# Optimization experiments

Hardware: AMD Instinct MI355X
Metric: run time of the kernel (lower is better)

## Reference

```python
import jax, jax.numpy as jnp
import numpy as np

BN_EPS = 1e-5


def gcn_conv(x, src, dst, W, b):
    # PyG GCNConv: add self-loops, symmetric normalization, bias after aggregation
    n = x.shape[0]
    h = x @ W                                   # [N, d]
    deg = jnp.zeros((n,), x.dtype).at[dst].add(1.0) + 1.0  # in-degree + self-loop
    dinv = jax.lax.rsqrt(deg)
    norm = dinv[src] * dinv[dst]                # [E]
    agg = jnp.zeros_like(h).at[dst].add(h[src] * norm[:, None])
    agg = agg + h * (dinv * dinv)[:, None]      # self-loop messages
    return agg + b


def batchnorm(x, gamma, beta):
    mu = x.mean(0)
    var = x.var(0)  # biased, as torch BN training mode
    return (x - mu) * jax.lax.rsqrt(var + BN_EPS) * gamma + beta


def mha(x, w_in, b_in, w_out, b_out, n_heads=4):
    # torch nn.MultiheadAttention, input [L, N, E]
    L, N, d = x.shape
    hd = d // n_heads
    qkv = x @ w_in.T + b_in                     # [L, N, 3d]
    q, k, v = jnp.split(qkv, 3, axis=-1)
    rh = lambda t: t.reshape(L, N, n_heads, hd)
    q = rh(q) * (1.0 / np.sqrt(hd))
    k, v = rh(k), rh(v)
    scores = jnp.einsum('lnhd,mnhd->nhlm', q, k)
    a = jax.nn.softmax(scores, axis=-1)
    o = jnp.einsum('nhlm,mnhd->lnhd', a, v).reshape(L, N, d)
    return o @ w_out.T + b_out


def setup_inputs() -> dict:
    key = jax.random.key(0)
    N, d, E, L, R = 50000, 128, 400000, 3, 4
    ks = jax.random.split(key, 12)
    s = 1.0 / np.sqrt(d)
    return {
        'features': jax.random.normal(ks[0], (N, d), jnp.float32),
        'rel_emb': jax.random.normal(ks[1], (R, d), jnp.float32),
        'edge_index': jax.random.randint(ks[2], (R, 2, E), 0, N, dtype=jnp.int32),
        'W_gcn': jax.random.normal(ks[3], (L, d, d), jnp.float32) * s,
        'b_gcn': jnp.zeros((L, d), jnp.float32),
        'bn_gamma': jnp.ones((L - 1, d), jnp.float32),
        'bn_beta': jnp.zeros((L - 1, d), jnp.float32),
        'W_rt': jax.random.normal(ks[4], (L, d, d), jnp.float32) * s,
        'b_rt': jnp.zeros((L, d), jnp.float32),
        'attn_w_in': jax.random.normal(ks[5], (3 * d, d), jnp.float32) * s,
        'attn_b_in': jnp.zeros((3 * d,), jnp.float32),
        'attn_w_out': jax.random.normal(ks[6], (d, d), jnp.float32) * s,
        'attn_b_out': jnp.zeros((d,), jnp.float32),
        'alphas': jnp.full((4,), 0.95, jnp.float32),
        'fusion_q': jax.random.normal(ks[7], (d,), jnp.float32),
        'fusion_w': jax.random.normal(ks[8], (d, d), jnp.float32) * s,
        'fusion_b': jnp.zeros((d,), jnp.float32),
    }


def reference(features, rel_emb, edge_index, W_gcn, b_gcn, bn_gamma, bn_beta,
              W_rt, b_rt, attn_w_in, attn_b_in, attn_w_out, attn_b_out,
              alphas, fusion_q, fusion_w, fusion_b):
    L = W_gcn.shape[0]
    # RelationGCN unpacks rel_emb as (poi_r, s_r, d_r, n_r) and processes
    # relations in order (n, poi, s, d) -> permute to processing order.
    perm = jnp.array([3, 0, 1, 2])
    rels = rel_emb[perm]                # [4, d], order (n, poi, s, d)
    edges = edge_index[perm]            # [4, 2, E]
    embs = jnp.broadcast_to(features, (4,) + features.shape)  # all start at features

    def inner(emb, r, src, dst, Wg, bg, gamma, beta):
        h = gcn_conv(emb * r, src, dst, Wg, bg)
        return emb + jax.nn.leaky_relu(batchnorm(h, gamma, beta))

    for i in range(L - 1):
        embs = jax.vmap(inner, in_axes=(0, 0, 0, 0, None, None, None, None))(
            embs, rels, edges[:, 0], edges[:, 1],
            W_gcn[i], b_gcn[i], bn_gamma[i], bn_beta[i])
        rels = rels @ W_rt[i].T + b_rt[i]
        # dropout p=0.0 -> identity

    embs = jax.vmap(lambda e, r, s_, t_: gcn_conv(e * r, s_, t_, W_gcn[-1], b_gcn[-1]))(
        embs, rels, edges[:, 0], edges[:, 1])
    rels = rels @ W_rt[-1].T + b_rt[-1]

    # PM_Model mis-unpacks RelationGCN outputs (returned order n,poi,s,d as
    # poi,s,d,n). CrossLayer then stacks (n_emb, poi_emb, d_emb, s_emb) which in
    # true processing order is (d, n, s, poi):
    stk = jnp.stack([embs[3], embs[0], embs[2], embs[1]])  # [4, N, d]
    fusion = mha(stk, attn_w_in, attn_b_in, attn_w_out, attn_b_out)
    a = alphas  # [alpha_n, alpha_poi, alpha_d, alpha_s]
    n_f = fusion[0] * a[0] + (1 - a[0]) * stk[0]
    poi_f = fusion[1] * a[1] + (1 - a[1]) * stk[1]
    d_f = fusion[2] * a[2] + (1 - a[2]) * stk[2]
    s_f = fusion[3] * a[3] + (1 - a[3]) * stk[3]

    def score(f):
        return jnp.mean(jnp.sum(jax.nn.leaky_relu(f @ fusion_w.T + fusion_b) * fusion_q, axis=1))

    w = jax.nn.softmax(jnp.stack([score(n_f), score(poi_f), score(s_f), score(d_f)]))
    region = w[0] * n_f + w[1] * poi_f + w[2] * s_f + w[3] * d_f

    # Final multiplies use the same mis-unpacked rel names:
    # n_r<-rels[3](true d), poi_r<-rels[0](true n), s_r<-rels[1], d_r<-rels[2]
    return (region, region * rels[3], region * rels[0], region * rels[1], region * rels[2])
```

## Files before the change

### kernel.cpp

```cpp
#include <hip/hip_runtime.h>
#include <cstdio>

#define DD 128
#define NREL 4

using short8 = __attribute__((ext_vector_type(8))) short;
using f32x4  = __attribute__((ext_vector_type(4))) float;

struct PtrB4 { const unsigned short* p[4]; };
struct OutB4 { unsigned short* p[4]; };

__device__ __forceinline__ int edge_perm(int r) { return (r + 3) & 3; }

__device__ __forceinline__ float bf_lo(unsigned u) { return __uint_as_float(u << 16); }
__device__ __forceinline__ float bf_hi(unsigned u) { return __uint_as_float(u & 0xffff0000u); }
__device__ __forceinline__ float bfe(short s) {
  return __uint_as_float(((unsigned)(unsigned short)s) << 16);
}
__device__ __forceinline__ unsigned short f2bf(float f) {
  unsigned x = __float_as_uint(f);
  unsigned r = (x + 0x7fffu + ((x >> 16) & 1u)) >> 16;
  return (unsigned short)r;
}
__device__ __forceinline__ unsigned pack2(float a, float b) {
  return (unsigned)f2bf(a) | ((unsigned)f2bf(b) << 16);
}


__global__ void rels_init(const float* __restrict__ rel_emb, float* __restrict__ rels) {
  int t = threadIdx.x;
  int r = t >> 7, c = t & 127;
  rels[t] = rel_emb[edge_perm(r) * DD + c];
}

__global__ void rels_update(const float* __restrict__ rin, const float* __restrict__ Wrt,
                            const float* __restrict__ brt, float* __restrict__ rout) {
  int t = threadIdx.x;
  int r = t >> 7, j = t & 127;
  float s = brt[j];
  const float* wr = Wrt + j * DD;
  const float* xr = rin + r * DD;
  for (int c = 0; c < DD; ++c) s += xr[c] * wr[c];
  rout[t] = s;
}

__global__ void scale_w_bf(const float* __restrict__ rels_i, const float* __restrict__ Wg,
                           unsigned short* __restrict__ Wsb) {
  int i = blockIdx.x * 256 + threadIdx.x;
  int r = i >> 14, rem = i & 16383, j = rem >> 7, c = rem & 127;
  Wsb[i] = f2bf(rels_i[r * DD + c] * Wg[c * DD + j]);
}

__global__ void conv_w(const float* __restrict__ w_in, const float* __restrict__ w_out,
                       const float* __restrict__ w_fus, unsigned short* __restrict__ Wab) {
  int i = blockIdx.x * 256 + threadIdx.x;
  float v = (i < 49152) ? w_in[i] : (i < 65536 ? w_out[i - 49152] : w_fus[i - 65536]);
  Wab[i] = f2bf(v);
}

__global__ void conv_f2b(const float* __restrict__ in, unsigned* __restrict__ out2, size_t n4) {
  size_t i = (size_t)blockIdx.x * 256 + threadIdx.x;
  if (i < n4) {
    float4 v = ((const float4*)in)[i];
    out2[i * 2]     = pack2(v.x, v.y);
    out2[i * 2 + 1] = pack2(v.z, v.w);
  }
}


__global__ void count_deg(const int* __restrict__ ei, int* __restrict__ deg, int N, int E) {
  int r = blockIdx.y;
  int base = blockIdx.x * 1024 + threadIdx.x;
  const int* dsts = ei + (size_t)edge_perm(r) * 2 * E + E;
#pragma unroll
  for (int k = 0; k < 4; ++k) {
    int e = base + k * 256;
    if (e < E) atomicAdd(deg + (size_t)r * N + dsts[e], 1);
  }
}

__global__ void finalize_dinv(const int* __restrict__ deg, float* __restrict__ dinv, int total) {
  int i = blockIdx.x * 256 + threadIdx.x;
  if (i < total) dinv[i] = rsqrtf((float)deg[i] + 1.0f);
}

__global__ void scan_block(const int* __restrict__ deg, int* __restrict__ excl,
                           int* __restrict__ bsums, int n) {
  __shared__ int sh[256];
  int i = blockIdx.x * 256 + threadIdx.x;
  int v = (i < n) ? deg[i] : 0;
  sh[threadIdx.x] = v;
  __syncthreads();
  for (int st = 1; st < 256; st <<= 1) {
    int t = (threadIdx.x >= st) ? sh[threadIdx.x - st] : 0;
    __syncthreads();
    sh[threadIdx.x] += t;
    __syncthreads();
  }
  if (i < n) excl[i] = sh[threadIdx.x] - v;
  if (threadIdx.x == 255) bsums[blockIdx.x] = sh[255];
}

__global__ void scan_sums(int* __restrict__ bsums, int nb) {
  __shared__ int sh[1024];
  int v = (threadIdx.x < nb) ? bsums[threadIdx.x] : 0;
  sh[threadIdx.x] = v;
  __syncthreads();
  for (int st = 1; st < 1024; st <<= 1) {
    int t = (threadIdx.x >= st) ? sh[threadIdx.x - st] : 0;
    __syncthreads();
    sh[threadIdx.x] += t;
    __syncthreads();
  }
  if (threadIdx.x < nb) bsums[threadIdx.x] = sh[threadIdx.x] - v;
}

__global__ void scan_add(int* __restrict__ excl, int* __restrict__ cursor,
                         const int* __restrict__ bsums, int n) {
  int i = blockIdx.x * 256 + threadIdx.x;
  if (i < n) {
    int o = excl[i] + bsums[blockIdx.x];
    excl[i] = o;
    cursor[i] = o;
  }
}

__global__ void fill_edges(const int* __restrict__ ei, int* __restrict__ cursor,
                           int* __restrict__ srcbuf, int N, int E) {
  int r = blockIdx.y;
  int base = blockIdx.x * 1024 + threadIdx.x;
  const int* bp = ei + (size_t)edge_perm(r) * 2 * E;
  int s[4], d[4], pos[4];
#pragma unroll
  for (int k = 0; k < 4; ++k) {
    int e = base + k * 256;
    s[k] = (e < E) ? bp[e] : 0;
    d[k] = (e < E) ? bp[E + e] : 0;
  }
#pragma unroll
  for (int k = 0; k < 4; ++k) {
    int e = base + k * 256;
    if (e < E) pos[k] = atomicAdd(&cursor[r * N + d[k]], 1);
  }
#pragma unroll
  for (int k = 0; k < 4; ++k) {
    int e = base + k * 256;
    if (e < E) srcbuf[pos[k]] = r * N + s[k];
  }
}

template <int MODE>
__global__ __launch_bounds__(256) void gemm_ws(PtrB4 xs, PtrB4 wz, OutB4 ys,
                                               const float* __restrict__ bias,
                                               const float* __restrict__ dinv,
                                               const float* __restrict__ fq,
                                               float* __restrict__ S,
                                               PtrB4 stks,
                                               const float* __restrict__ alphas,
                                               int M) {
  int z = blockIdx.y;
  const unsigned short* __restrict__ X = xs.p[z];
  const unsigned short* __restrict__ W = wz.p[z];
  int tid = threadIdx.x;
  int wave = tid >> 6, lane = tid & 63;
  int r16 = lane & 15, kgrp = lane >> 4;
  int rowhalf = wave >> 1, colbase = (wave & 1) * 64;
  int blockrow = blockIdx.x * 64;

  short8 b[4][4];
#pragma unroll
  for (int s = 0; s < 4; ++s)
#pragma unroll
    for (int cn = 0; cn < 4; ++cn)
      b[s][cn] = *(const short8*)(W + ((colbase + cn * 16 + r16) << 7) + s * 32 + kgrp * 8);

  int row0 = blockrow + rowhalf * 32 + r16;
  int r0c = row0 < M ? row0 : M - 1;
  int r1c = row0 + 16 < M ? row0 + 16 : M - 1;
  short8 a[2][4];
#pragma unroll
  for (int s = 0; s < 4; ++s) {
    a[0][s] = *(const short8*)(X + (size_t)r0c * DD + s * 32 + kgrp * 8);
    a[1][s] = *(const short8*)(X + (size_t)r1c * DD + s * 32 + kgrp * 8);
  }

  f32x4 acc[2][4];
#pragma unroll
  for (int rt = 0; rt < 2; ++rt)
#pragma unroll
    for (int cn = 0; cn < 4; ++cn)
#pragma unroll
      for (int j = 0; j < 4; ++j) acc[rt][cn][j] = 0.f;

#pragma unroll
  for (int s = 0; s < 4; ++s)
#pragma unroll
    for (int rt = 0; rt < 2; ++rt)
#pragma unroll
      for (int cn = 0; cn < 4; ++cn)
        acc[rt][cn] = __builtin_amdgcn_mfma_f32_16x16x32_bf16(a[rt][s], b[s][cn], acc[rt][cn], 0, 0, 0);

  __shared__ float red[256];
  if constexpr (MODE == 2) {
    float ss = 0.f;
#pragma unroll
    for (int rt = 0; rt < 2; ++rt)
#pragma unroll
      for (int cn = 0; cn < 4; ++cn) {
        int col = colbase + cn * 16 + r16;
        float bb = bias[col];
        float qc = fq[col];
#pragma unroll
        for (int i = 0; i < 4; ++i) {
          int row = blockrow + rowhalf * 32 + rt * 16 + kgrp * 4 + i;
          if (row < M) {
            float y = acc[rt][cn][i] + bb;
            float v = y > 0.f ? y : 0.01f * y;
            ss += v * qc;
          }
        }
      }
    red[tid] = ss;
    __syncthreads();
    for (int st = 128; st > 0; st >>= 1) {
      if (tid < st) red[tid] += red[tid + st];
      __syncthreads();
    }
    if (tid == 0) atomicAdd(S + z, red[0]);
  } else {
    __shared__ __align__(16) unsigned short tile[64][DD + 8];
    float dv[2][4];
    if constexpr (MODE == 0) {
#pragma unroll
      for (int rt = 0; rt < 2; ++rt)
#pragma unroll
        for (int i = 0; i < 4; ++i) {
          int row = blockrow + rowhalf * 32 + rt * 16 + kgrp * 4 + i;
          dv[rt][i] = dinv[(size_t)z * M + (row < M ? row : 0)];
        }
    }
#pragma unroll
    for (int rt = 0; rt < 2; ++rt)
#pragma unroll
      for (int cn = 0; cn < 4; ++cn) {
        int col = colbase + cn * 16 + r16;
        float bb = (MODE == 1 || MODE == 3) ? bias[col] : 0.f;
#pragma unroll
        for (int i = 0; i < 4; ++i) {
          int wrow = rowhalf * 32 + rt * 16 + kgrp * 4 + i;
          float y = acc[rt][cn][i] + bb;
          if constexpr (MODE == 0) y *= dv[rt][i];
          tile[wrow][col] = f2bf(y);
        }
      }
    __syncthreads();
    int orow = tid >> 2, seg = tid & 3;
    int grow = blockrow + orow;
    if (grow < M) {
      unsigned short* Yp = ys.p[z] + (size_t)grow * DD + seg * 32;
      const unsigned short* tp = &tile[orow][seg * 32];
      if constexpr (MODE == 3) {
        float aa = alphas[z], na = 1.f - aa;
        const unsigned short* sp = stks.p[z] + (size_t)grow * DD + seg * 32;
#pragma unroll
        for (int k = 0; k < 4; ++k) {
          uint4 pv = *(const uint4*)(tp + k * 8);
          uint4 sv = *(const uint4*)(sp + k * 8);
          const unsigned* pw = &pv.x;
          const unsigned* sw = &sv.x;
          uint4 o; unsigned* ow = &o.x;
#pragma unroll
          for (int j = 0; j < 4; ++j)
            ow[j] = pack2(aa * bf_lo(pw[j]) + na * bf_lo(sw[j]),
                          aa * bf_hi(pw[j]) + na * bf_hi(sw[j]));
          *(uint4*)(Yp + k * 8) = o;
        }
      } else {
#pragma unroll
        for (int k = 0; k < 4; ++k)
          *(uint4*)(Yp + k * 8) = *(const uint4*)(tp + k * 8);
      }
    }
  }
}

template <int WB>
__global__ __launch_bounds__(256) void gemm_upd(PtrB4 res, PtrB4 abs_, PtrB4 wz,
                                                OutB4 xout, OutB4 ys,
                                                const float* __restrict__ ssx,
                                                const float* __restrict__ dinv, int M) {
  int z = blockIdx.y;
  const unsigned short* __restrict__ R = res.p[z];
  const unsigned short* __restrict__ A = abs_.p[z];
  const unsigned short* __restrict__ W = wz.p[z];
  int tid = threadIdx.x;

  __shared__ float ssc[DD], ssh[DD];
  if (tid < DD) {
    ssc[tid] = ssx[((size_t)z * DD + tid) * 2];
    ssh[tid] = ssx[((size_t)z * DD + tid) * 2 + 1];
  }
  __syncthreads();

  int wave = tid >> 6, lane = tid & 63;
  int r16 = lane & 15, kgrp = lane >> 4;
  int rowhalf = wave >> 1, colbase = (wave & 1) * 64;
  int blockrow = blockIdx.x * 64;

  short8 b[4][4];
#pragma unroll
  for (int s = 0; s < 4; ++s)
#pragma unroll
    for (int cn = 0; cn < 4; ++cn)
      b[s][cn] = *(const short8*)(W + ((colbase + cn * 16 + r16) << 7) + s * 32 + kgrp * 8);

  int row0 = blockrow + rowhalf * 32 + r16;
  int rc[2];
  rc[0] = row0 < M ? row0 : M - 1;
  rc[1] = row0 + 16 < M ? row0 + 16 : M - 1;
  short8 a[2][4];
#pragma unroll
  for (int rt = 0; rt < 2; ++rt)
#pragma unroll
    for (int s = 0; s < 4; ++s) {
      int cbase = s * 32 + kgrp * 8;
      short8 rv = *(const short8*)(R + (size_t)rc[rt] * DD + cbase);
      short8 av = *(const short8*)(A + (size_t)rc[rt] * DD + cbase);
      short8 av2;
#pragma unroll
      for (int j = 0; j < 8; ++j) {
        float x = bfe(av[j]) * ssc[cbase + j] + ssh[cbase + j];
        x = x > 0.f ? x : 0.01f * x;
        av2[j] = (short)f2bf(bfe(rv[j]) + x);
      }
      a[rt][s] = av2;
    }
  if (WB) {
#pragma unroll
    for (int rt = 0; rt < 2; ++rt) {
      int row = row0 + rt * 16;
      if (row < M) {
#pragma unroll
        for (int s = 0; s < 4; ++s)
          *(short8*)(xout.p[z] + (size_t)row * DD + s * 32 + kgrp * 8) = a[rt][s];
      }
    }
  }

  f32x4 acc[2][4];
#pragma unroll
  for (int rt = 0; rt < 2; ++rt)
#pragma unroll
    for (int cn = 0; cn < 4; ++cn)
#pragma unroll
      for (int j = 0; j < 4; ++j) acc[rt][cn][j] = 0.f;
#pragma unroll
  for (int s = 0; s < 4; ++s)
#pragma unroll
    for (int rt = 0; rt < 2; ++rt)
#pragma unroll
      for (int cn = 0; cn < 4; ++cn)
        acc[rt][cn] = __builtin_amdgcn_mfma_f32_16x16x32_bf16(a[rt][s], b[s][cn], acc[rt][cn], 0, 0, 0);

  __shared__ __align__(16) unsigned short tile[64][DD + 8];
  float dv[2][4];
#pragma unroll
  for (int rt = 0; rt < 2; ++rt)
#pragma unroll
    for (int i = 0; i < 4; ++i) {
      int row = blockrow + rowhalf * 32 + rt * 16 + kgrp * 4 + i;
      dv[rt][i] = dinv[(size_t)z * M + (row < M ? row : 0)];
    }
#pragma unroll
  for (int rt = 0; rt < 2; ++rt)
#pragma unroll
    for (int cn = 0; cn < 4; ++cn) {
      int col = colbase + cn * 16 + r16;
#pragma unroll
      for (int i = 0; i < 4; ++i) {
        int wrow = rowhalf * 32 + rt * 16 + kgrp * 4 + i;
        tile[wrow][col] = f2bf(acc[rt][cn][i] * dv[rt][i]);
      }
    }
  __syncthreads();
  int orow = tid >> 2, seg = tid & 3;
  int grow = blockrow + orow;
  if (grow < M) {
    unsigned short* Yp = ys.p[z] + (size_t)grow * DD + seg * 32;
    const unsigned short* tp = &tile[orow][seg * 32];
#pragma unroll
    for (int k = 0; k < 4; ++k)
      *(uint4*)(Yp + k * 8) = *(const uint4*)(tp + k * 8);
  }
}

__global__ __launch_bounds__(256) void gather_agg(const int* __restrict__ srcbuf,
                                                  const int* __restrict__ offs,
                                                  const int* __restrict__ deg,
                                                  const float* __restrict__ dinv,
                                                  const uint2* __restrict__ Bs2,
                                                  const float* __restrict__ bias,
                                                  uint2* __restrict__ Ab2, int N4) {
  int rn = blockIdx.x * 8 + (threadIdx.x >> 5);
  if (rn >= N4) return;
  int lane = threadIdx.x & 31;
  int st = offs[rn], cnt = deg[rn];
  uint2 u = Bs2[(size_t)rn * 32 + lane];
  float a0 = bf_lo(u.x), a1 = bf_hi(u.x), a2 = bf_lo(u.y), a3 = bf_hi(u.y);
  int e = 0;
  for (; e + 8 <= cnt; e += 8) {
    int rr[8];
#pragma unroll
    for (int j = 0; j < 8; ++j) rr[j] = srcbuf[st + e + j];
    uint2 vv[8];
#pragma unroll
    for (int j = 0; j < 8; ++j) vv[j] = Bs2[(size_t)rr[j] * 32 + lane];
#pragma unroll
    for (int j = 0; j < 8; ++j) {
      a0 += bf_lo(vv[j].x); a1 += bf_hi(vv[j].x);
      a2 += bf_lo(vv[j].y); a3 += bf_hi(vv[j].y);
    }
  }
  if (e + 4 <= cnt) {
    int rr[4];
#pragma unroll
    for (int j = 0; j < 4; ++j) rr[j] = srcbuf[st + e + j];
    uint2 vv[4];
#pragma unroll
    for (int j = 0; j < 4; ++j) vv[j] = Bs2[(size_t)rr[j] * 32 + lane];
#pragma unroll
    for (int j = 0; j < 4; ++j) {
      a0 += bf_lo(vv[j].x); a1 += bf_hi(vv[j].x);
      a2 += bf_lo(vv[j].y); a3 += bf_hi(vv[j].y);
    }
    e += 4;
  }
  for (; e < cnt; ++e) {
    uint2 v = Bs2[(size_t)srcbuf[st + e] * 32 + lane];
    a0 += bf_lo(v.x); a1 += bf_hi(v.x); a2 += bf_lo(v.y); a3 += bf_hi(v.y);
  }
  float dvv = dinv[rn];
  int c = lane * 4;
  uint2 o;
  o.x = pack2(a0 * dvv + bias[c],     a1 * dvv + bias[c + 1]);
  o.y = pack2(a2 * dvv + bias[c + 2], a3 * dvv + bias[c + 3]);
  Ab2[(size_t)rn * 32 + lane] = o;
}


__global__ void bn_stats(const unsigned* __restrict__ Ab2, float* __restrict__ sums, int N) {
  int r = blockIdx.y;
  int lane = threadIdx.x & 63, grp = threadIdx.x >> 6;
  float s0 = 0.f, q0 = 0.f, s1 = 0.f, q1 = 0.f;
  const unsigned* base = Ab2 + (size_t)r * N * 64;
  for (int n = blockIdx.x * 4 + grp; n < N; n += gridDim.x * 4) {
    unsigned u = base[(size_t)n * 64 + lane];
    float a = bf_lo(u), b = bf_hi(u);
    s0 += a; q0 += a * a; s1 += b; q1 += b * b;
  }
  __shared__ float sh[4][64][4];
  sh[grp][lane][0] = s0; sh[grp][lane][1] = q0; sh[grp][lane][2] = s1; sh[grp][lane][3] = q1;
  __syncthreads();
  if (grp == 0) {
#pragma unroll
    for (int g = 1; g < 4; ++g) {
      s0 += sh[g][lane][0]; q0 += sh[g][lane][1]; s1 += sh[g][lane][2]; q1 += sh[g][lane][3];
    }
    int c0 = lane * 2;
    atomicAdd(sums + (r * DD + c0) * 2, s0);
    atomicAdd(sums + (r * DD + c0) * 2 + 1, q0);
    atomicAdd(sums + (r * DD + c0 + 1) * 2, s1);
    atomicAdd(sums + (r * DD + c0 + 1) * 2 + 1, q1);
  }
}

__global__ void bn_final(const float* __restrict__ sums, const float* __restrict__ gamma,
                         const float* __restrict__ beta, float* __restrict__ ss, int N) {
  int t = threadIdx.x;
  int c = t & 127;
  float mu = sums[t * 2] / N;
  float var = sums[t * 2 + 1] / N - mu * mu;
  float sc = gamma[c] * rsqrtf(var + 1e-5f);
  ss[t * 2] = sc;
  ss[t * 2 + 1] = beta[c] - mu * sc;
}

__global__ void attn_fused(const unsigned short* __restrict__ Q,
                           const unsigned short* __restrict__ K,
                           const unsigned short* __restrict__ V,
                           unsigned* __restrict__ Ob2, int N) {
  int sb = threadIdx.x >> 6;
  int node = blockIdx.x * 4 + sb;
  int lane = threadIdx.x & 63;
  __shared__ float qs[4][4][132], ks[4][4][132], vs[4][4][132];
  __shared__ float ps[4][64];
  if (node < N) {
    int l = lane >> 4, c8 = (lane & 15) * 8;
    uint4 qv = *(const uint4*)(Q + ((size_t)l * N + node) * DD + c8);
    uint4 kv = *(const uint4*)(K + ((size_t)l * N + node) * DD + c8);
    uint4 vv = *(const uint4*)(V + ((size_t)l * N + node) * DD + c8);
    unsigned qa[4] = {qv.x, qv.y, qv.z, qv.w};
    unsigned ka[4] = {kv.x, kv.y, kv.z, kv.w};
    unsigned va[4] = {vv.x, vv.y, vv.z, vv.w};
#pragma unroll
    for (int j = 0; j < 4; ++j) {
      qs[sb][l][c8 + 2 * j]     = bf_lo(qa[j]);
      qs[sb][l][c8 + 2 * j + 1] = bf_hi(qa[j]);
      ks[sb][l][c8 + 2 * j]     = bf_lo(ka[j]);
      ks[sb][l][c8 + 2 * j + 1] = bf_hi(ka[j]);
      vs[sb][l][c8 + 2 * j]     = bf_lo(va[j]);
      vs[sb][l][c8 + 2 * j + 1] = bf_hi(va[j]);
    }
  }
  __syncthreads();
  if (node < N) {
    int h = lane >> 4, l = (lane >> 2) & 3, m = lane & 3;
    const float* qp = &qs[sb][l][h * 32];
    const float* kp = &ks[sb][m][h * 32];
    float s = 0.f;
#pragma unroll
    for (int k2 = 0; k2 < 32; ++k2) s += qp[k2] * kp[k2];
    s *= 0.17677669529663687f;
    float mx = s;
    mx = fmaxf(mx, __shfl_xor(mx, 1));
    mx = fmaxf(mx, __shfl_xor(mx, 2));
    float e = expf(s - mx);
    float sum = e;
    sum += __shfl_xor(sum, 1);
    sum += __shfl_xor(sum, 2);
    ps[sb][lane] = e / sum;
  }
  __syncthreads();
  if (node < N) {
    int c0 = lane * 2, h = c0 >> 5;
    const float* pp = &ps[sb][h * 16];
#pragma unroll
    for (int l = 0; l < 4; ++l) {
      float ol = pp[l * 4 + 0] * vs[sb][0][c0] + pp[l * 4 + 1] * vs[sb][1][c0] +
                 pp[l * 4 + 2] * vs[sb][2][c0] + pp[l * 4 + 3] * vs[sb][3][c0];
      float oh = pp[l * 4 + 0] * vs[sb][0][c0 + 1] + pp[l * 4 + 1] * vs[sb][1][c0 + 1] +
                 pp[l * 4 + 2] * vs[sb][2][c0 + 1] + pp[l * 4 + 3] * vs[sb][3][c0 + 1];
      Ob2[((size_t)l * N + node) * 64 + lane] = pack2(ol, oh);
    }
  }
}

__global__ void wcoef(const float* __restrict__ S, float* __restrict__ coef, int N) {
  if (threadIdx.x == 0) {
    float v0 = S[0] / N, v1 = S[1] / N, v2 = S[3] / N, v3 = S[2] / N;
    float mx = fmaxf(fmaxf(v0, v1), fmaxf(v2, v3));
    float e0 = expf(v0 - mx), e1 = expf(v1 - mx), e2 = expf(v2 - mx), e3 = expf(v3 - mx);
    float inv = 1.f / (e0 + e1 + e2 + e3);
    coef[0] = e0 * inv; coef[1] = e1 * inv; coef[2] = e3 * inv; coef[3] = e2 * inv;
  }
}

__device__ __forceinline__ float bfat(uint2 u, int j) {
  unsigned w = (j < 2) ? u.x : u.y;
  return (j & 1) ? bf_hi(w) : bf_lo(w);
}

__global__ void final_out(const unsigned short* __restrict__ fb, const float* __restrict__ coef,
                          const float* __restrict__ rels3, float* __restrict__ out, int N) {
  size_t NK = (size_t)N * DD;
  size_t i4 = (size_t)blockIdx.x * 256 + threadIdx.x;
  if (i4 >= NK / 4) return;
  size_t g = i4 * 4;
  int c = (int)(g & 127);
  float c0 = coef[0], c1 = coef[1], c2 = coef[2], c3 = coef[3];
  uint2 u0 = *(const uint2*)(fb + g);
  uint2 u1 = *(const uint2*)(fb + NK + g);
  uint2 u2 = *(const uint2*)(fb + 2 * NK + g);
  uint2 u3 = *(const uint2*)(fb + 3 * NK + g);
  float4 reg4, o1, o2, o3, o4;
  float* rp = &reg4.x; float* p1 = &o1.x; float* p2 = &o2.x; float* p3 = &o3.x; float* p4 = &o4.x;
#pragma unroll
  for (int j = 0; j < 4; ++j) {
    float region = c0 * bfat(u0, j) + c1 * bfat(u1, j) + c2 * bfat(u2, j) + c3 * bfat(u3, j);
    rp[j] = region;
    p1[j] = region * rels3[3 * DD + c + j];
    p2[j] = region * rels3[0 * DD + c + j];
    p3[j] = region * rels3[1 * DD + c + j];
    p4[j] = region * rels3[2 * DD + c + j];
  }
  *(float4*)(out + g) = reg4;
  *(float4*)(out + NK + g) = o1;
  *(float4*)(out + 2 * NK + g) = o2;
  *(float4*)(out + 3 * NK + g) = o3;
  *(float4*)(out + 4 * NK + g) = o4;
}


extern "C" void kernel_launch(void* const* d_in, const int* in_sizes, int n_in,
                              void* d_out, int out_size, void* d_ws, size_t ws_size,
                              hipStream_t stream) {
  const float* features  = (const float*)d_in[0];
  const float* rel_emb   = (const float*)d_in[1];
  const int*   edge_idx  = (const int*)d_in[2];
  const float* W_gcn     = (const float*)d_in[3];
  const float* b_gcn     = (const float*)d_in[4];
  const float* bn_gamma  = (const float*)d_in[5];
  const float* bn_beta   = (const float*)d_in[6];
  const float* W_rt      = (const float*)d_in[7];
  const float* b_rt      = (const float*)d_in[8];
  const float* attn_w_in = (const float*)d_in[9];
  const float* attn_b_in = (const float*)d_in[10];
  const float* attn_wout = (const float*)d_in[11];
  const float* attn_bout = (const float*)d_in[12];
  const float* alphas    = (const float*)d_in[13];
  const float* fusion_q  = (const float*)d_in[14];
  const float* fusion_w  = (const float*)d_in[15];
  const float* fusion_b  = (const float*)d_in[16];

  int N = in_sizes[0] / DD;
  int E = in_sizes[2] / (2 * NREL);
  size_t NK = (size_t)N * DD;
  int N4 = 4 * N;

  unsigned short* Xb = (unsigned short*)d_ws;
  unsigned short* Bs = Xb + 4 * NK;
  unsigned short* Ab = Bs + 4 * NK;
  unsigned short* Ub = Ab + 4 * NK;
  unsigned short* Fb = Ub + 4 * NK;
  float* dinv  = (float*)(Fb + NK);
  unsigned short* Wgcnb = (unsigned short*)(dinv + N4);
  unsigned short* Wab   = Wgcnb + 4 * DD * DD;
  float* rels  = (float*)(Wab + 5 * DD * DD);
  float* bnsum = rels + 4 * 512;
  float* bnss  = bnsum + 1024;
  float* S     = bnss + 1024;
  float* coef  = S + 4;
  int* deg_i   = (int*)(coef + 4);
  int* offs    = deg_i + N4;
  int* cur     = offs + N4;
  int* bsums   = cur + N4;
  int* srcb    = bsums + 1024;

  size_t needed = (size_t)((char*)(srcb + 4 * E) - (char*)d_ws);
  if (ws_size < needed) {
    fprintf(stderr, "kernel_launch: ws too small (%zu < %zu)\n", ws_size, needed);
    return;
  }

  int gemmGrid = (N + 63) / 64;
  int scanBlocks = (N4 + 255) / 256;
  int egrid4 = (E + 1023) / 1024;

  hipMemsetAsync(deg_i, 0, (size_t)N4 * sizeof(int), stream);
  count_deg<<<dim3(egrid4, 4), 256, 0, stream>>>(edge_idx, deg_i, N, E);
  finalize_dinv<<<scanBlocks, 256, 0, stream>>>(deg_i, dinv, N4);
  scan_block<<<scanBlocks, 256, 0, stream>>>(deg_i, offs, bsums, N4);
  scan_sums<<<1, 1024, 0, stream>>>(bsums, scanBlocks);
  scan_add<<<scanBlocks, 256, 0, stream>>>(offs, cur, bsums, N4);
  fill_edges<<<dim3(egrid4, 4), 256, 0, stream>>>(edge_idx, cur, srcb, N, E);

  rels_init<<<1, 512, 0, stream>>>(rel_emb, rels);
  conv_w<<<5 * 16384 / 256, 256, 0, stream>>>(attn_w_in, attn_wout, fusion_w, Wab);
  conv_f2b<<<(int)((NK / 4 + 255) / 256), 256, 0, stream>>>(features, (unsigned*)Fb, NK / 4);

  PtrB4 wz, abIn, resIn, dummyP;
  OutB4 msgOut, xbOut, dummyO;
  for (int r = 0; r < 4; ++r) {
    wz.p[r] = Wgcnb + (size_t)r * DD * DD;
    abIn.p[r] = Ab + (size_t)r * NK;
    msgOut.p[r] = Bs + (size_t)r * NK;
    xbOut.p[r] = Xb + (size_t)r * NK;
    dummyP.p[r] = nullptr;
    dummyO.p[r] = nullptr;
  }
  const float* dummy = nullptr;

  scale_w_bf<<<256, 256, 0, stream>>>(rels, W_gcn, Wgcnb);
  {
    PtrB4 xs; for (int r = 0; r < 4; ++r) xs.p[r] = Fb;
    gemm_ws<0><<<dim3(gemmGrid, 4), 256, 0, stream>>>(xs, wz, msgOut, dummy, dinv, dummy,
                                                      nullptr, dummyP, dummy, N);
  }
  gather_agg<<<(N4 + 7) / 8, 256, 0, stream>>>(srcb, offs, deg_i, dinv, (const uint2*)Bs,
                                               b_gcn, (uint2*)Ab, N4);
  hipMemsetAsync(bnsum, 0, 1024 * sizeof(float), stream);
  bn_stats<<<dim3(128, 4), 256, 0, stream>>>((const unsigned*)Ab, bnsum, N);
  bn_final<<<1, 512, 0, stream>>>(bnsum, bn_gamma, bn_beta, bnss, N);
  rels_update<<<1, 512, 0, stream>>>(rels, W_rt, b_rt, rels + 512);

  scale_w_bf<<<256, 256, 0, stream>>>(rels + 512, W_gcn + (size_t)DD * DD, Wgcnb);
  for (int r = 0; r < 4; ++r) resIn.p[r] = Fb;
  gemm_upd<1><<<dim3(gemmGrid, 4), 256, 0, stream>>>(resIn, abIn, wz, xbOut, msgOut,
                                                     bnss, dinv, N);
  gather_agg<<<(N4 + 7) / 8, 256, 0, stream>>>(srcb, offs, deg_i, dinv, (const uint2*)Bs,
                                               b_gcn + DD, (uint2*)Ab, N4);
  hipMemsetAsync(bnsum, 0, 1024 * sizeof(float), stream);
  bn_stats<<<dim3(128, 4), 256, 0, stream>>>((const unsigned*)Ab, bnsum, N);
  bn_final<<<1, 512, 0, stream>>>(bnsum, bn_gamma + DD, bn_beta + DD, bnss, N);
  rels_update<<<1, 512, 0, stream>>>(rels + 512, W_rt + (size_t)DD * DD, b_rt + DD, rels + 1024);

  scale_w_bf<<<256, 256, 0, stream>>>(rels + 1024, W_gcn + (size_t)2 * DD * DD, Wgcnb);
  for (int r = 0; r < 4; ++r) resIn.p[r] = Xb + (size_t)r * NK;
  gemm_upd<0><<<dim3(gemmGrid, 4), 256, 0, stream>>>(resIn, abIn, wz, dummyO, msgOut,
                                                     bnss, dinv, N);
  gather_agg<<<(N4 + 7) / 8, 256, 0, stream>>>(srcb, offs, deg_i, dinv, (const uint2*)Bs,
                                               b_gcn + 2 * DD, (uint2*)Ab, N4);
  rels_update<<<1, 512, 0, stream>>>(rels + 1024, W_rt + (size_t)2 * DD * DD, b_rt + 2 * DD,
                                     rels + 1536);

  const int pstk[4] = {3, 0, 2, 1};
  PtrB4 stk, fromO, fromF, w4;
  OutB4 toQ, toK, toV, toF;
  for (int l = 0; l < 4; ++l) {
    stk.p[l] = Ab + (size_t)pstk[l] * NK;
    toQ.p[l] = Xb + (size_t)l * NK;
    toK.p[l] = Bs + (size_t)l * NK;
    toV.p[l] = Ub + (size_t)l * NK;
    toF.p[l] = Bs + (size_t)l * NK;
    fromO.p[l] = Xb + (size_t)l * NK;
    fromF.p[l] = Bs + (size_t)l * NK;
  }

  for (int l = 0; l < 4; ++l) w4.p[l] = Wab;
  gemm_ws<1><<<dim3(gemmGrid, 4), 256, 0, stream>>>(stk, w4, toQ, attn_b_in, dummy, dummy,
                                                    nullptr, dummyP, dummy, N);
  for (int l = 0; l < 4; ++l) w4.p[l] = Wab + 16384;
  gemm_ws<1><<<dim3(gemmGrid, 4), 256, 0, stream>>>(stk, w4, toK, attn_b_in + DD, dummy, dummy,
                                                    nullptr, dummyP, dummy, N);
  for (int l = 0; l < 4; ++l) w4.p[l] = Wab + 2 * 16384;
  gemm_ws<1><<<dim3(gemmGrid, 4), 256, 0, stream>>>(stk, w4, toV, attn_b_in + 2 * DD, dummy,
                                                    dummy, nullptr, dummyP, dummy, N);
  attn_fused<<<(N + 3) / 4, 256, 0, stream>>>(Xb, Bs, Ub, (unsigned*)Xb, N);
  for (int l = 0; l < 4; ++l) w4.p[l] = Wab + 3 * 16384;
  gemm_ws<3><<<dim3(gemmGrid, 4), 256, 0, stream>>>(fromO, w4, toF, attn_bout, dummy, dummy,
                                                    nullptr, stk, alphas, N);
  hipMemsetAsync(S, 0, 4 * sizeof(float), stream);
  for (int l = 0; l < 4; ++l) w4.p[l] = Wab + 4 * 16384;
  gemm_ws<2><<<dim3(gemmGrid, 4), 256, 0, stream>>>(fromF, w4, toQ , fusion_b, dummy,
                                                    fusion_q, S, dummyP, dummy, N);
  wcoef<<<1, 64, 0, stream>>>(S, coef, N);
  final_out<<<(int)((NK / 4 + 255) / 256), 256, 0, stream>>>(Bs, coef, rels + 1536,
                                                             (float*)d_out, N);
}
```

Before: 1.031 ms.

## Stage GEMM weights in LDS and give each wave a full-width 16-row tile

Both GEMM kernels now copy the 128x128 bf16 weight tile into shared memory once per block with a padded row stride. Each wave then computes a 16x128 output slab, reading B fragments from LDS instead of holding a 64-column slice of B in registers. This cuts per-thread register use and the redundant global weight loads across waves, at the cost of LDS reads per MFMA and an extra barrier before the shared buffer is reused as the output tile. The bn_stats grid is also enlarged for more parallelism.

```diff
diff --git a/kernel.cpp b/kernel.cpp
--- a/kernel.cpp
+++ b/kernel.cpp
@@ -150,76 +150,75 @@
 }
 
 template <int MODE>
-__global__ __launch_bounds__(256) void gemm_ws(PtrB4 xs, PtrB4 wz, OutB4 ys,
-                                               const float* __restrict__ bias,
-                                               const float* __restrict__ dinv,
-                                               const float* __restrict__ fq,
-                                               float* __restrict__ S,
-                                               PtrB4 stks,
-                                               const float* __restrict__ alphas,
-                                               int M) {
+__global__ __launch_bounds__(256) void gemm_lds(PtrB4 xs, PtrB4 wz, OutB4 ys,
+                                                const float* __restrict__ bias,
+                                                const float* __restrict__ dinv,
+                                                const float* __restrict__ fq,
+                                                float* __restrict__ S,
+                                                PtrB4 stks,
+                                                const float* __restrict__ alphas,
+                                                int M) {
   int z = blockIdx.y;
   const unsigned short* __restrict__ X = xs.p[z];
   const unsigned short* __restrict__ W = wz.p[z];
   int tid = threadIdx.x;
+
+  __shared__ __align__(16) char smem[128 * 134 * 2];
+  unsigned short (*Bl)[134] = (unsigned short (*)[134])smem;
+  unsigned short (*tile)[136] = (unsigned short (*)[136])smem;
+
+  {
+    int row = tid >> 1, off = (tid & 1) * 64;
+    const unsigned short* Wr = W + (row << 7) + off;
+#pragma unroll
+    for (int k = 0; k < 8; ++k)
+      *(short8*)&Bl[row][off + k * 8] = *(const short8*)(Wr + k * 8);
+  }
+  __syncthreads();
+
   int wave = tid >> 6, lane = tid & 63;
   int r16 = lane & 15, kgrp = lane >> 4;
-  int rowhalf = wave >> 1, colbase = (wave & 1) * 64;
   int blockrow = blockIdx.x * 64;
-
-  short8 b[4][4];
+  int rowA = blockrow + wave * 16 + r16;
+  int rowAc = rowA < M ? rowA : M - 1;
+
+  short8 a[4];
 #pragma unroll
   for (int s = 0; s < 4; ++s)
-#pragma unroll
-    for (int cn = 0; cn < 4; ++cn)
-      b[s][cn] = *(const short8*)(W + ((colbase + cn * 16 + r16) << 7) + s * 32 + kgrp * 8);
-
-  int row0 = blockrow + rowhalf * 32 + r16;
-  int r0c = row0 < M ? row0 : M - 1;
-  int r1c = row0 + 16 < M ? row0 + 16 : M - 1;
-  short8 a[2][4];
-#pragma unroll
-  for (int s = 0; s < 4; ++s) {
-    a[0][s] = *(const short8*)(X + (size_t)r0c * DD + s * 32 + kgrp * 8);
-    a[1][s] = *(const short8*)(X + (size_t)r1c * DD + s * 32 + kgrp * 8);
-  }
-
-  f32x4 acc[2][4];
-#pragma unroll
-  for (int rt = 0; rt < 2; ++rt)
-#pragma unroll
-    for (int cn = 0; cn < 4; ++cn)
-#pragma unroll
-      for (int j = 0; j < 4; ++j) acc[rt][cn][j] = 0.f;
+    a[s] = *(const short8*)(X + (size_t)rowAc * DD + s * 32 + kgrp * 8);
+
+  f32x4 acc[8];
+#pragma unroll
+  for (int nt = 0; nt < 8; ++nt)
+#pragma unroll
+    for (int j = 0; j < 4; ++j) acc[nt][j] = 0.f;
 
 #pragma unroll
   for (int s = 0; s < 4; ++s)
 #pragma unroll
-    for (int rt = 0; rt < 2; ++rt)
-#pragma unroll
-      for (int cn = 0; cn < 4; ++cn)
-        acc[rt][cn] = __builtin_amdgcn_mfma_f32_16x16x32_bf16(a[rt][s], b[s][cn], acc[rt][cn], 0, 0, 0);
-
-  __shared__ float red[256];
+    for (int nt = 0; nt < 8; ++nt) {
+      short8 b = *(const short8*)&Bl[nt * 16 + r16][s * 32 + kgrp * 8];
+      acc[nt] = __builtin_amdgcn_mfma_f32_16x16x32_bf16(a[s], b, acc[nt], 0, 0, 0);
+    }
+
   if constexpr (MODE == 2) {
+    __shared__ float red[256];
     float ss = 0.f;
 #pragma unroll
-    for (int rt = 0; rt < 2; ++rt)
-#pragma unroll
-      for (int cn = 0; cn < 4; ++cn) {
-        int col = colbase + cn * 16 + r16;
-        float bb = bias[col];
-        float qc = fq[col];
-#pragma unroll
-        for (int i = 0; i < 4; ++i) {
-          int row = blockrow + rowhalf * 32 + rt * 16 + kgrp * 4 + i;
-          if (row < M) {
-            float y = acc[rt][cn][i] + bb;
-            float v = y > 0.f ? y : 0.01f * y;
-            ss += v * qc;
-          }
+    for (int nt = 0; nt < 8; ++nt) {
+      int col = nt * 16 + r16;
+      float bb = bias[col];
+      float qc = fq[col];
+#pragma unroll
+      for (int i = 0; i < 4; ++i) {
+        int row = blockrow + wave * 16 + kgrp * 4 + i;
+        if (row < M) {
+          float y = acc[nt][i] + bb;
+          float v = y > 0.f ? y : 0.01f * y;
+          ss += v * qc;
         }
       }
+    }
     red[tid] = ss;
     __syncthreads();
     for (int st = 128; st > 0; st >>= 1) {
@@ -228,31 +227,27 @@
     }
     if (tid == 0) atomicAdd(S + z, red[0]);
   } else {
-    __shared__ __align__(16) unsigned short tile[64][DD + 8];
-    float dv[2][4];
+    float dv[4];
     if constexpr (MODE == 0) {
 #pragma unroll
-      for (int rt = 0; rt < 2; ++rt)
-#pragma unroll
-        for (int i = 0; i < 4; ++i) {
-          int row = blockrow + rowhalf * 32 + rt * 16 + kgrp * 4 + i;
-          dv[rt][i] = dinv[(size_t)z * M + (row < M ? row : 0)];
-        }
-    }
-#pragma unroll
-    for (int rt = 0; rt < 2; ++rt)
-#pragma unroll
-      for (int cn = 0; cn < 4; ++cn) {
-        int col = colbase + cn * 16 + r16;
-        float bb = (MODE == 1 || MODE == 3) ? bias[col] : 0.f;
-#pragma unroll
-        for (int i = 0; i < 4; ++i) {
-          int wrow = rowhalf * 32 + rt * 16 + kgrp * 4 + i;
-          float y = acc[rt][cn][i] + bb;
-          if constexpr (MODE == 0) y *= dv[rt][i];
-          tile[wrow][col] = f2bf(y);
-        }
+      for (int i = 0; i < 4; ++i) {
+        int row = blockrow + wave * 16 + kgrp * 4 + i;
+        dv[i] = dinv[(size_t)z * M + (row < M ? row : 0)];
       }
+    }
+    __syncthreads();
+#pragma unroll
+    for (int nt = 0; nt < 8; ++nt) {
+      int col = nt * 16 + r16;
+      float bb = (MODE == 1 || MODE == 3) ? bias[col] : 0.f;
+#pragma unroll
+      for (int i = 0; i < 4; ++i) {
+        int wrow = wave * 16 + kgrp * 4 + i;
+        float y = acc[nt][i] + bb;
+        if constexpr (MODE == 0) y *= dv[i];
+        tile[wrow][col] = f2bf(y);
+      }
+    }
     __syncthreads();
     int orow = tid >> 2, seg = tid & 3;
     int grow = blockrow + orow;
@@ -295,7 +290,18 @@
   const unsigned short* __restrict__ W = wz.p[z];
   int tid = threadIdx.x;
 
+  __shared__ __align__(16) char smem[128 * 134 * 2];
+  unsigned short (*Bl)[134] = (unsigned short (*)[134])smem;
+  unsigned short (*tile)[136] = (unsigned short (*)[136])smem;
   __shared__ float ssc[DD], ssh[DD];
+
+  {
+    int row = tid >> 1, off = (tid & 1) * 64;
+    const unsigned short* Wr = W + (row << 7) + off;
+#pragma unroll
+    for (int k = 0; k < 8; ++k)
+      *(short8*)&Bl[row][off + k * 8] = *(const short8*)(Wr + k * 8);
+  }
   if (tid < DD) {
     ssc[tid] = ssx[((size_t)z * DD + tid) * 2];
     ssh[tid] = ssx[((size_t)z * DD + tid) * 2 + 1];
@@ -304,84 +310,60 @@
 
   int wave = tid >> 6, lane = tid & 63;
   int r16 = lane & 15, kgrp = lane >> 4;
-  int rowhalf = wave >> 1, colbase = (wave & 1) * 64;
   int blockrow = blockIdx.x * 64;
-
-  short8 b[4][4];
+  int rowA = blockrow + wave * 16 + r16;
+  int rowAc = rowA < M ? rowA : M - 1;
+
+  short8 a[4];
+#pragma unroll
+  for (int s = 0; s < 4; ++s) {
+    int cbase = s * 32 + kgrp * 8;
+    short8 rv = *(const short8*)(R + (size_t)rowAc * DD + cbase);
+    short8 av = *(const short8*)(A + (size_t)rowAc * DD + cbase);
+    short8 av2;
+#pragma unroll
+    for (int j = 0; j < 8; ++j) {
+      float x = bfe(av[j]) * ssc[cbase + j] + ssh[cbase + j];
+      x = x > 0.f ? x : 0.01f * x;
+      av2[j] = (short)f2bf(bfe(rv[j]) + x);
+    }
+    a[s] = av2;
+  }
+  if (WB && rowA < M) {
+#pragma unroll
+    for (int s = 0; s < 4; ++s)
+      *(short8*)(xout.p[z] + (size_t)rowA * DD + s * 32 + kgrp * 8) = a[s];
+  }
+
+  f32x4 acc[8];
+#pragma unroll
+  for (int nt = 0; nt < 8; ++nt)
+#pragma unroll
+    for (int j = 0; j < 4; ++j) acc[nt][j] = 0.f;
 #pragma unroll
   for (int s = 0; s < 4; ++s)
 #pragma unroll
-    for (int cn = 0; cn < 4; ++cn)
-      b[s][cn] = *(const short8*)(W + ((colbase + cn * 16 + r16) << 7) + s * 32 + kgrp * 8);
-
-  int row0 = blockrow + rowhalf * 32 + r16;
-  int rc[2];
-  rc[0] = row0 < M ? row0 : M - 1;
-  rc[1] = row0 + 16 < M ? row0 + 16 : M - 1;
-  short8 a[2][4];
-#pragma unroll
-  for (int rt = 0; rt < 2; ++rt)
-#pragma unroll
-    for (int s = 0; s < 4; ++s) {
-      int cbase = s * 32 + kgrp * 8;
-      short8 rv = *(const short8*)(R + (size_t)rc[rt] * DD + cbase);
-      short8 av = *(const short8*)(A + (size_t)rc[rt] * DD + cbase);
-      short8 av2;
-#pragma unroll
-      for (int j = 0; j < 8; ++j) {
-        float x = bfe(av[j]) * ssc[cbase + j] + ssh[cbase + j];
-        x = x > 0.f ? x : 0.01f * x;
-        av2[j] = (short)f2bf(bfe(rv[j]) + x);
-      }
-      a[rt][s] = av2;
-    }
-  if (WB) {
-#pragma unroll
-    for (int rt = 0; rt < 2; ++rt) {
-      int row = row0 + rt * 16;
-      if (row < M) {
-#pragma unroll
-        for (int s = 0; s < 4; ++s)
-          *(short8*)(xout.p[z] + (size_t)row * DD + s * 32 + kgrp * 8) = a[rt][s];
-      }
-    }
-  }
-
-  f32x4 acc[2][4];
-#pragma unroll
-  for (int rt = 0; rt < 2; ++rt)
-#pragma unroll
-    for (int cn = 0; cn < 4; ++cn)
-#pragma unroll
-      for (int j = 0; j < 4; ++j) acc[rt][cn][j] = 0.f;
-#pragma unroll
-  for (int s = 0; s < 4; ++s)
-#pragma unroll
-    for (int rt = 0; rt < 2; ++rt)
-#pragma unroll
-      for (int cn = 0; cn < 4; ++cn)
-        acc[rt][cn] = __builtin_amdgcn_mfma_f32_16x16x32_bf16(a[rt][s], b[s][cn], acc[rt][cn], 0, 0, 0);
-
-  __shared__ __align__(16) unsigned short tile[64][DD + 8];
-  float dv[2][4];
-#pragma unroll
-  for (int rt = 0; rt < 2; ++rt)
+    for (int nt = 0; nt < 8; ++nt) {
+      short8 b = *(const short8*)&Bl[nt * 16 + r16][s * 32 + kgrp * 8];
+      acc[nt] = __builtin_amdgcn_mfma_f32_16x16x32_bf16(a[s], b, acc[nt], 0, 0, 0);
+    }
+
+  float dv[4];
+#pragma unroll
+  for (int i = 0; i < 4; ++i) {
+    int row = blockrow + wave * 16 + kgrp * 4 + i;
+    dv[i] = dinv[(size_t)z * M + (row < M ? row : 0)];
+  }
+  __syncthreads();
+#pragma unroll
+  for (int nt = 0; nt < 8; ++nt) {
+    int col = nt * 16 + r16;
 #pragma unroll
     for (int i = 0; i < 4; ++i) {
-      int row = blockrow + rowhalf * 32 + rt * 16 + kgrp * 4 + i;
-      dv[rt][i] = dinv[(size_t)z * M + (row < M ? row : 0)];
-    }
-#pragma unroll
-  for (int rt = 0; rt < 2; ++rt)
-#pragma unroll
-    for (int cn = 0; cn < 4; ++cn) {
-      int col = colbase + cn * 16 + r16;
-#pragma unroll
-      for (int i = 0; i < 4; ++i) {
-        int wrow = rowhalf * 32 + rt * 16 + kgrp * 4 + i;
-        tile[wrow][col] = f2bf(acc[rt][cn][i] * dv[rt][i]);
-      }
-    }
+      int wrow = wave * 16 + kgrp * 4 + i;
+      tile[wrow][col] = f2bf(acc[nt][i] * dv[i]);
+    }
+  }
   __syncthreads();
   int orow = tid >> 2, seg = tid & 3;
   int grow = blockrow + orow;
@@ -673,13 +655,13 @@
   scale_w_bf<<<256, 256, 0, stream>>>(rels, W_gcn, Wgcnb);
   {
     PtrB4 xs; for (int r = 0; r < 4; ++r) xs.p[r] = Fb;
-    gemm_ws<0><<<dim3(gemmGrid, 4), 256, 0, stream>>>(xs, wz, msgOut, dummy, dinv, dummy,
-                                                      nullptr, dummyP, dummy, N);
+    gemm_lds<0><<<dim3(gemmGrid, 4), 256, 0, stream>>>(xs, wz, msgOut, dummy, dinv, dummy,
+                                                       nullptr, dummyP, dummy, N);
   }
   gather_agg<<<(N4 + 7) / 8, 256, 0, stream>>>(srcb, offs, deg_i, dinv, (const uint2*)Bs,
                                                b_gcn, (uint2*)Ab, N4);
   hipMemsetAsync(bnsum, 0, 1024 * sizeof(float), stream);
-  bn_stats<<<dim3(128, 4), 256, 0, stream>>>((const unsigned*)Ab, bnsum, N);
+  bn_stats<<<dim3(400, 4), 256, 0, stream>>>((const unsigned*)Ab, bnsum, N);
   bn_final<<<1, 512, 0, stream>>>(bnsum, bn_gamma, bn_beta, bnss, N);
   rels_update<<<1, 512, 0, stream>>>(rels, W_rt, b_rt, rels + 512);
 
@@ -690,7 +672,7 @@
   gather_agg<<<(N4 + 7) / 8, 256, 0, stream>>>(srcb, offs, deg_i, dinv, (const uint2*)Bs,
                                                b_gcn + DD, (uint2*)Ab, N4);
   hipMemsetAsync(bnsum, 0, 1024 * sizeof(float), stream);
-  bn_stats<<<dim3(128, 4), 256, 0, stream>>>((const unsigned*)Ab, bnsum, N);
+  bn_stats<<<dim3(400, 4), 256, 0, stream>>>((const unsigned*)Ab, bnsum, N);
   bn_final<<<1, 512, 0, stream>>>(bnsum, bn_gamma + DD, bn_beta + DD, bnss, N);
   rels_update<<<1, 512, 0, stream>>>(rels + 512, W_rt + (size_t)DD * DD, b_rt + DD, rels + 1024);
 
@@ -717,22 +699,22 @@
   }
 
   for (int l = 0; l < 4; ++l) w4.p[l] = Wab;
-  gemm_ws<1><<<dim3(gemmGrid, 4), 256, 0, stream>>>(stk, w4, toQ, attn_b_in, dummy, dummy,
-                                                    nullptr, dummyP, dummy, N);
+  gemm_lds<1><<<dim3(gemmGrid, 4), 256, 0, stream>>>(stk, w4, toQ, attn_b_in, dummy, dummy,
+                                                     nullptr, dummyP, dummy, N);
   for (int l = 0; l < 4; ++l) w4.p[l] = Wab + 16384;
-  gemm_ws<1><<<dim3(gemmGrid, 4), 256, 0, stream>>>(stk, w4, toK, attn_b_in + DD, dummy, dummy,
-                                                    nullptr, dummyP, dummy, N);
+  gemm_lds<1><<<dim3(gemmGrid, 4), 256, 0, stream>>>(stk, w4, toK, attn_b_in + DD, dummy, dummy,
+                                                     nullptr, dummyP, dummy, N);
   for (int l = 0; l < 4; ++l) w4.p[l] = Wab + 2 * 16384;
-  gemm_ws<1><<<dim3(gemmGrid, 4), 256, 0, stream>>>(stk, w4, toV, attn_b_in + 2 * DD, dummy,
-                                                    dummy, nullptr, dummyP, dummy, N);
+  gemm_lds<1><<<dim3(gemmGrid, 4), 256, 0, stream>>>(stk, w4, toV, attn_b_in + 2 * DD, dummy,
+                                                     dummy, nullptr, dummyP, dummy, N);
   attn_fused<<<(N + 3) / 4, 256, 0, stream>>>(Xb, Bs, Ub, (unsigned*)Xb, N);
   for (int l = 0; l < 4; ++l) w4.p[l] = Wab + 3 * 16384;
-  gemm_ws<3><<<dim3(gemmGrid, 4), 256, 0, stream>>>(fromO, w4, toF, attn_bout, dummy, dummy,
-                                                    nullptr, stk, alphas, N);
+  gemm_lds<3><<<dim3(gemmGrid, 4), 256, 0, stream>>>(fromO, w4, toF, attn_bout, dummy, dummy,
+                                                     nullptr, stk, alphas, N);
   hipMemsetAsync(S, 0, 4 * sizeof(float), stream);
   for (int l = 0; l < 4; ++l) w4.p[l] = Wab + 4 * 16384;
-  gemm_ws<2><<<dim3(gemmGrid, 4), 256, 0, stream>>>(fromF, w4, toQ , fusion_b, dummy,
-                                                    fusion_q, S, dummyP, dummy, N);
+  gemm_lds<2><<<dim3(gemmGrid, 4), 256, 0, stream>>>(fromF, w4, toQ , fusion_b, dummy,
+                                                     fusion_q, S, dummyP, dummy, N);
   wcoef<<<1, 64, 0, stream>>>(S, coef, N);
   final_out<<<(int)((NK / 4 + 255) / 256), 256, 0, stream>>>(Bs, coef, rels + 1536,
                                                              (float*)d_out, N);
```

New measurement: 1.163 ms. 1.13x slower.
